# Performance work log

Hardware: AMD Instinct MI355X
Metric: run time of the kernel (lower is better)

## Reference

```python
import jax, jax.numpy as jnp
import numpy as np

NUM_EMBEDDINGS = 1024
EMBEDDING_DIM = 64
COMMITMENT_WEIGHT = 0.25
BATCH = 262144


def setup_inputs() -> dict:
    key = jax.random.key(0)
    k1, k2 = jax.random.split(key)
    z = jax.random.normal(k1, (BATCH, EMBEDDING_DIM), dtype=jnp.float32)
    # torch init: uniform_(-1/K, 1/K)
    bound = 1.0 / NUM_EMBEDDINGS
    codebook = jax.random.uniform(k2, (NUM_EMBEDDINGS, EMBEDDING_DIM), dtype=jnp.float32,
                                  minval=-bound, maxval=bound)
    return {"z": z, "codebook": codebook}


def reference(z, codebook):
    # distances[b, k] = ||z_b||^2 - 2 z_b . c_k + ||c_k||^2   -> [B, K]
    z2 = jnp.sum(z * z, axis=1, keepdims=True)                 # [B, 1]
    c2 = jnp.sum(codebook * codebook, axis=1)                  # [K]
    cross = jnp.matmul(z, codebook.T)                          # [B, K]
    distances = z2 - 2.0 * cross + c2
    indices = jnp.argmin(distances, axis=1)                    # [B]
    # original uses one-hot @ codebook; direct gather is the same math
    z_q = codebook[indices]                                    # [B, D]
    commitment_loss = jnp.mean((jax.lax.stop_gradient(z_q) - z) ** 2)
    codebook_loss = jnp.mean((z_q - jax.lax.stop_gradient(z)) ** 2)
    vq_loss = codebook_loss + COMMITMENT_WEIGHT * commitment_loss
    # straight-through estimator
    z_q_st = z + jax.lax.stop_gradient(z_q - z)
    return z_q_st, vq_loss, indices
```

## Files before the change

### kernel.cpp

```cpp
#include <hip/hip_runtime.h>

#define BATCH   262144
#define NCODE   1024
#define DIM     64
#define BLOCK   256
#define NBLK    (BATCH / BLOCK)
#define MARGIN2 2e-5f
#define QCAP    65536


typedef __attribute__((ext_vector_type(8))) short bf16x8;
typedef __attribute__((ext_vector_type(4))) float f32x4;

#define MFMA(a, b, c) __builtin_amdgcn_mfma_f32_16x16x32_bf16(a, b, c, 0, 0, 0)

__device__ __forceinline__ void split1(float f, unsigned short& h, unsigned short& l) {
    unsigned u = __float_as_uint(f);
    unsigned r = (u + 0x7fffu + ((u >> 16) & 1u)) >> 16;
    h = (unsigned short)r;
    float hf = __uint_as_float(r << 16);
    float lo = f - hf;
    unsigned u2 = __float_as_uint(lo);
    l = (unsigned short)((u2 + 0x7fffu + ((u2 >> 16) & 1u)) >> 16);
}

__global__ __launch_bounds__(256) void prep_kernel(
        const float* __restrict__ cb, float* __restrict__ c2, float* __restrict__ c2n,
        float* __restrict__ cbT, unsigned short* __restrict__ pack,
        unsigned int* __restrict__ qcount)
{
    const int gid = blockIdx.x * 256 + threadIdx.x;
    if (gid == 0) *qcount = 0u;
    cbT[(size_t)(gid & 63) * NCODE + (gid >> 6)] = cb[gid];
    if (gid < NCODE) {
        const float* row = cb + (size_t)gid * DIM;
        float r[8];
#pragma unroll
        for (int j = 0; j < 8; ++j) r[j] = __fmul_rn(row[j], row[j]);
#pragma unroll
        for (int i = 8; i < DIM; i += 8) {
#pragma unroll
            for (int j = 0; j < 8; ++j) r[j] = __fadd_rn(r[j], __fmul_rn(row[i + j], row[i + j]));
        }
        const float v = __fadd_rn(__fadd_rn(__fadd_rn(r[0], r[1]), __fadd_rn(r[2], r[3])),
                                  __fadd_rn(__fadd_rn(r[4], r[5]), __fadd_rn(r[6], r[7])));
        c2[gid] = v;
        c2n[gid] = -0.5f * v;
    }
    if (gid < 4096) {
        const int t = gid >> 6, lane = gid & 63;
        const int c = t * 16 + (lane & 15);
        const int g = lane >> 4;
#pragma unroll
        for (int s = 0; s < 2; ++s) {
            const float* src = cb + (size_t)c * DIM + s * 32 + g * 8;
            bf16x8 hv, lv;
#pragma unroll
            for (int j = 0; j < 8; ++j) {
                unsigned short hh, ll; split1(src[j], hh, ll);
                hv[j] = (short)hh; lv[j] = (short)ll;
            }
            *(bf16x8*)(pack + ((size_t)(t * 4 + 2 * s + 0) * 64 + lane) * 8) = hv;
            *(bf16x8*)(pack + ((size_t)(t * 4 + 2 * s + 1) * 64 + lane) * 8) = lv;
        }
    }
}

__global__ __launch_bounds__(256) void screen_kernel(
        const float* __restrict__ z, const unsigned short* __restrict__ pack,
        const float* __restrict__ c2n, float* __restrict__ out_idx,
        int* __restrict__ queue, unsigned int* __restrict__ qcount)
{
    __shared__ __align__(16) unsigned short lds[2][8192];
    const int tid  = threadIdx.x;
    const int lane = tid & 63, wid = tid >> 6;
    const int col  = lane & 15, g = lane >> 4;
    const int rowbase = blockIdx.x * 128 + wid * 32;

    bf16x8 Ah[2][2], Al[2][2];
#pragma unroll
    for (int rt = 0; rt < 2; ++rt)
#pragma unroll
        for (int s = 0; s < 2; ++s) {
            const float* zp = z + (size_t)(rowbase + rt * 16 + col) * DIM + s * 32 + g * 8;
            float tmp[8];
            *(float4*)(tmp)     = ((const float4*)zp)[0];
            *(float4*)(tmp + 4) = ((const float4*)zp)[1];
            bf16x8 hv, lv;
#pragma unroll
            for (int j = 0; j < 8; ++j) {
                unsigned short hh, ll; split1(tmp[j], hh, ll);
                hv[j] = (short)hh; lv[j] = (short)ll;
            }
            Ah[rt][s] = hv; Al[rt][s] = lv;
        }

    float b1[8], b2[8], bk[8];
#pragma unroll
    for (int i = 0; i < 8; ++i) {
        b1[i] = -__builtin_inff(); b2[i] = -__builtin_inff(); bk[i] = 0.f;
    }
    float codef = (float)col;

#define UPD(i, sv) { const float s_ = (sv); \
                     bk[i] = (s_ > b1[i]) ? codef : bk[i]; \
                     b2[i] = __builtin_amdgcn_fmed3f(s_, b1[i], b2[i]); \
                     b1[i] = fmaxf(b1[i], s_); }

#define STAGE(c, buf) { \
_Pragma("unroll") \
        for (int i_ = 0; i_ < 4; ++i_) { \
            const int seg_ = wid * 4 + i_; \
            const unsigned short* g_ = pack + (size_t)(c) * 8192 + seg_ * 512 + lane * 8; \
            unsigned short* l_ = &lds[buf][seg_ * 512]; \
            __builtin_amdgcn_global_load_lds( \
                (const __attribute__((address_space(1))) unsigned int*)g_, \
                (__attribute__((address_space(3))) unsigned int*)l_, 16, 0, 0); \
        } }

    int cur = 0;
    STAGE(0, 0);
    __syncthreads();
#pragma unroll 1
    for (int c = 0; c < 16; ++c) {
        if (c < 15) STAGE(c + 1, cur ^ 1);
        float c2r[4];
#pragma unroll
        for (int u = 0; u < 4; ++u) c2r[u] = c2n[(c * 4 + u) * 16 + col];
        const unsigned short* buf = &lds[cur][0];
#pragma unroll
        for (int u = 0; u < 4; ++u) {
            const unsigned short* lb = buf + u * 2048;
            bf16x8 Bh0 = *(const bf16x8*)(lb +    0 + lane * 8);
            bf16x8 Bl0 = *(const bf16x8*)(lb +  512 + lane * 8);
            bf16x8 Bh1 = *(const bf16x8*)(lb + 1024 + lane * 8);
            bf16x8 Bl1 = *(const bf16x8*)(lb + 1536 + lane * 8);
            const float cv = c2r[u];
#pragma unroll
            for (int rt = 0; rt < 2; ++rt) {
                f32x4 acc = {cv, cv, cv, cv};
                acc = MFMA(Ah[rt][0], Bh0, acc); acc = MFMA(Ah[rt][1], Bh1, acc);
                acc = MFMA(Ah[rt][0], Bl0, acc); acc = MFMA(Al[rt][0], Bh0, acc);
                acc = MFMA(Ah[rt][1], Bl1, acc); acc = MFMA(Al[rt][1], Bh1, acc);
#pragma unroll
                for (int reg = 0; reg < 4; ++reg) UPD(rt * 4 + reg, acc[reg]);
            }
            codef += 16.f;
        }
        __syncthreads();
        cur ^= 1;
    }
#undef UPD
#undef STAGE

#pragma unroll
    for (int i = 0; i < 8; ++i) {
        float v1 = b1[i], v2 = b2[i], vk = bk[i];
#pragma unroll
        for (int m = 1; m < 16; m <<= 1) {
            const float o1 = __shfl_xor(v1, m);
            const float o2 = __shfl_xor(v2, m);
            const float ok = __shfl_xor(vk, m);
            v2 = fmaxf(fmaxf(v2, o2), fminf(v1, o1));
            if (o1 > v1) vk = ok;
            v1 = fmaxf(v1, o1);
        }
        if (col == 0) {
            const int rt = i >> 2, reg = i & 3;
            const int row = rowbase + rt * 16 + g * 4 + reg;
            out_idx[row] = vk;
            if (v1 - v2 <= MARGIN2) {
                unsigned int p = atomicAdd(qcount, 1u);
                if (p < QCAP) queue[p] = row;
            }
        }
    }
}

__device__ void fix_row(int row, const float* __restrict__ z, const float* __restrict__ cbT,
                        const float* __restrict__ c2, float* __restrict__ out_idx,
                        float* zs, float* rv, int* ri)
{
    const int tid = threadIdx.x;
    __syncthreads();
    if (tid < 16) ((float4*)zs)[tid] = ((const float4*)(z + (size_t)row * DIM))[tid];
    __syncthreads();
    float ra[8];
#pragma unroll
    for (int j = 0; j < 8; ++j) ra[j] = __fmul_rn(zs[j], zs[j]);
#pragma unroll
    for (int d = 8; d < DIM; d += 8) {
#pragma unroll
        for (int j = 0; j < 8; ++j) ra[j] = __fadd_rn(ra[j], __fmul_rn(zs[d + j], zs[d + j]));
    }
    const float z2 = __fadd_rn(__fadd_rn(__fadd_rn(ra[0], ra[1]), __fadd_rn(ra[2], ra[3])),
                               __fadd_rn(__fadd_rn(ra[4], ra[5]), __fadd_rn(ra[6], ra[7])));
    float a[4] = {0.f, 0.f, 0.f, 0.f};
#pragma unroll 8
    for (int d = 0; d < DIM; ++d) {
        const float zd = zs[d];
        const float4 cv = ((const float4*)(cbT + (size_t)d * NCODE))[tid];
        a[0] = __fmaf_rn(zd, cv.x, a[0]);
        a[1] = __fmaf_rn(zd, cv.y, a[1]);
        a[2] = __fmaf_rn(zd, cv.z, a[2]);
        a[3] = __fmaf_rn(zd, cv.w, a[3]);
    }
    const int k0 = tid * 4;
    float best = __builtin_inff();
    int bestk = NCODE;
#pragma unroll
    for (int j = 0; j < 4; ++j) {
        const float dist = __fadd_rn(__fmaf_rn(-2.0f, a[j], z2), c2[k0 + j]);
        if (dist < best) { best = dist; bestk = k0 + j; }
    }
    rv[tid] = best; ri[tid] = bestk;
    __syncthreads();
#pragma unroll
    for (int s = 128; s > 0; s >>= 1) {
        if (tid < s) {
            const float ov = rv[tid + s]; const int oi = ri[tid + s];
            if (ov < rv[tid] || (ov == rv[tid] && oi < ri[tid])) { rv[tid] = ov; ri[tid] = oi; }
        }
        __syncthreads();
    }
    if (tid == 0) out_idx[row] = (float)ri[0];
}

__global__ __launch_bounds__(256) void fix_kernel(
        const float* __restrict__ z, const float* __restrict__ cbT,
        const float* __restrict__ c2, const int* __restrict__ queue,
        const unsigned int* __restrict__ qcount, float* __restrict__ out_idx)
{
    __shared__ float zs[DIM];
    __shared__ float rv[256];
    __shared__ int   ri[256];
    const unsigned int nq = *qcount;
    if (nq <= QCAP) {
        for (unsigned int qi = blockIdx.x; qi < nq; qi += gridDim.x)
            fix_row(queue[qi], z, cbT, c2, out_idx, zs, rv, ri);
    } else {
        for (int row = blockIdx.x; row < BATCH; row += (int)gridDim.x)
            fix_row(row, z, cbT, c2, out_idx, zs, rv, ri);
    }
}

__global__ __launch_bounds__(BLOCK) void emit_kernel(
        const float* __restrict__ z, const float* __restrict__ cb,
        const float* __restrict__ out_idx, float* __restrict__ out_zq,
        double* __restrict__ partial)
{
    const int b = blockIdx.x * BLOCK + threadIdx.x;
    const int bestk = (int)out_idx[b];
    const float* cq = cb + (size_t)bestk * DIM;
    const float4* zv = (const float4*)(z + (size_t)b * DIM);
    const float4* qv = (const float4*)cq;
    float4* ov = (float4*)(out_zq + (size_t)b * DIM);
    double lsum = 0.0;
#pragma unroll
    for (int i = 0; i < DIM / 4; ++i) {
        float4 qq = qv[i], zl = zv[i];
        float qa[4] = {qq.x, qq.y, qq.z, qq.w};
        float za[4] = {zl.x, zl.y, zl.z, zl.w};
        float o[4];
#pragma unroll
        for (int j = 0; j < 4; ++j) {
            const float t = __fsub_rn(qa[j], za[j]);
            o[j] = __fadd_rn(za[j], t);
            lsum += (double)t * (double)t;
        }
        float4 vv; vv.x = o[0]; vv.y = o[1]; vv.z = o[2]; vv.w = o[3];
        ov[i] = vv;
    }

    __shared__ double sred[BLOCK];
    sred[threadIdx.x] = lsum;
    __syncthreads();
#pragma unroll
    for (int s = BLOCK / 2; s > 0; s >>= 1) {
        if (threadIdx.x < s) sred[threadIdx.x] += sred[threadIdx.x + s];
        __syncthreads();
    }
    if (threadIdx.x == 0) partial[blockIdx.x] = sred[0];
}

__global__ void loss_kernel(const double* __restrict__ partial, float* __restrict__ out_loss) {
    __shared__ double sred[256];
    double s = 0.0;
    for (int i = threadIdx.x; i < NBLK; i += 256) s += partial[i];
    sred[threadIdx.x] = s;
    __syncthreads();
#pragma unroll
    for (int st = 128; st > 0; st >>= 1) {
        if (threadIdx.x < st) sred[threadIdx.x] += sred[threadIdx.x + st];
        __syncthreads();
    }
    if (threadIdx.x == 0) {
        const double mean = sred[0] / (double)((size_t)BATCH * DIM);
        const float L = (float)mean;
        out_loss[0] = __fadd_rn(L, __fmul_rn(0.25f, L));
    }
}

extern "C" void kernel_launch(void* const* d_in, const int* in_sizes, int n_in,
                              void* d_out, int out_size, void* d_ws, size_t ws_size,
                              hipStream_t stream) {
    (void)in_sizes; (void)n_in; (void)out_size; (void)ws_size;
    const float* z  = (const float*)d_in[0];
    const float* cb = (const float*)d_in[1];
    float* out      = (float*)d_out;
    float* out_zq   = out;
    float* out_loss = out + (size_t)BATCH * DIM;
    float* out_idx  = out + (size_t)BATCH * DIM + 1;
    double* partial = (double*)d_ws;
    float* c2       = (float*)((char*)d_ws + 8192);
    unsigned int* qcount = (unsigned int*)((char*)d_ws + 12288);
    float* c2n      = (float*)((char*)d_ws + 12544);
    unsigned short* pack = (unsigned short*)((char*)d_ws + 16640);
    int* queue      = (int*)((char*)d_ws + 278784);
    float* cbT      = (float*)((char*)d_ws + 540928);

    prep_kernel<<<256, 256, 0, stream>>>(cb, c2, c2n, cbT, pack, qcount);
    screen_kernel<<<BATCH / 128, 256, 0, stream>>>(z, pack, c2n, out_idx, queue, qcount);
    fix_kernel<<<2048, 256, 0, stream>>>(z, cbT, c2, queue, qcount, out_idx);
    emit_kernel<<<NBLK, BLOCK, 0, stream>>>(z, cb, out_idx, out_zq, partial);
    loss_kernel<<<1, 256, 0, stream>>>(partial, out_loss);
}
```

Before: 307.1 us.

## Stream codebook tiles from global into registers and fuse loss reduction into emit

The screen kernel no longer stages codebook tiles through double-buffered LDS with barriers. Each wave now loads its B fragments straight from global/L2 into registers, ping-ponging between two register sets, and it sets a launch-bounds occupancy hint. The separate loss kernel is removed: emit blocks atomically add their partial sums into a double accumulator, and the last block to finish writes the loss, which saves one launch. This trades LDS traffic and syncs for redundant global reads of the codebook by every wave, and the atomic double summation order becomes nondeterministic.

```diff
diff --git a/kernel.cpp b/kernel.cpp
--- a/kernel.cpp
+++ b/kernel.cpp
@@ -27,10 +27,11 @@
 __global__ __launch_bounds__(256) void prep_kernel(
         const float* __restrict__ cb, float* __restrict__ c2, float* __restrict__ c2n,
         float* __restrict__ cbT, unsigned short* __restrict__ pack,
-        unsigned int* __restrict__ qcount)
+        unsigned int* __restrict__ qcount, double* __restrict__ dsum,
+        unsigned int* __restrict__ dcount)
 {
     const int gid = blockIdx.x * 256 + threadIdx.x;
-    if (gid == 0) *qcount = 0u;
+    if (gid == 0) { *qcount = 0u; *dsum = 0.0; *dcount = 0u; }
     cbT[(size_t)(gid & 63) * NCODE + (gid >> 6)] = cb[gid];
     if (gid < NCODE) {
         const float* row = cb + (size_t)gid * DIM;
@@ -66,12 +67,11 @@
     }
 }
 
-__global__ __launch_bounds__(256) void screen_kernel(
+__global__ __launch_bounds__(256, 4) void screen_kernel(
         const float* __restrict__ z, const unsigned short* __restrict__ pack,
         const float* __restrict__ c2n, float* __restrict__ out_idx,
         int* __restrict__ queue, unsigned int* __restrict__ qcount)
 {
-    __shared__ __align__(16) unsigned short lds[2][8192];
     const int tid  = threadIdx.x;
     const int lane = tid & 63, wid = tid >> 6;
     const int col  = lane & 15, g = lane >> 4;
@@ -107,51 +107,37 @@
                      b2[i] = __builtin_amdgcn_fmed3f(s_, b1[i], b2[i]); \
                      b1[i] = fmaxf(b1[i], s_); }
 
-#define STAGE(c, buf) { \
+#define LOADB(BUF, t) { const unsigned short* p_ = pack + (size_t)(t) * 2048 + lane * 8; \
+        BUF[0] = *(const bf16x8*)(p_);        BUF[1] = *(const bf16x8*)(p_ +  512); \
+        BUF[2] = *(const bf16x8*)(p_ + 1024); BUF[3] = *(const bf16x8*)(p_ + 1536); }
+
+#define COMPUTE(BUF, cv) { \
 _Pragma("unroll") \
-        for (int i_ = 0; i_ < 4; ++i_) { \
-            const int seg_ = wid * 4 + i_; \
-            const unsigned short* g_ = pack + (size_t)(c) * 8192 + seg_ * 512 + lane * 8; \
-            unsigned short* l_ = &lds[buf][seg_ * 512]; \
-            __builtin_amdgcn_global_load_lds( \
-                (const __attribute__((address_space(1))) unsigned int*)g_, \
-                (__attribute__((address_space(3))) unsigned int*)l_, 16, 0, 0); \
-        } }
-
-    int cur = 0;
-    STAGE(0, 0);
-    __syncthreads();
+    for (int rt = 0; rt < 2; ++rt) { \
+        f32x4 acc = {cv, cv, cv, cv}; \
+        acc = MFMA(Ah[rt][0], BUF[0], acc); acc = MFMA(Ah[rt][1], BUF[2], acc); \
+        acc = MFMA(Ah[rt][0], BUF[1], acc); acc = MFMA(Al[rt][0], BUF[0], acc); \
+        acc = MFMA(Ah[rt][1], BUF[3], acc); acc = MFMA(Al[rt][1], BUF[2], acc); \
+_Pragma("unroll") \
+        for (int reg = 0; reg < 4; ++reg) UPD(rt * 4 + reg, acc[reg]); \
+    } \
+    codef += 16.f; }
+
+    bf16x8 BA[4], BB[4];
+    float cA, cB;
+    LOADB(BA, 0); cA = c2n[col];
 #pragma unroll 1
-    for (int c = 0; c < 16; ++c) {
-        if (c < 15) STAGE(c + 1, cur ^ 1);
-        float c2r[4];
-#pragma unroll
-        for (int u = 0; u < 4; ++u) c2r[u] = c2n[(c * 4 + u) * 16 + col];
-        const unsigned short* buf = &lds[cur][0];
-#pragma unroll
-        for (int u = 0; u < 4; ++u) {
-            const unsigned short* lb = buf + u * 2048;
-            bf16x8 Bh0 = *(const bf16x8*)(lb +    0 + lane * 8);
-            bf16x8 Bl0 = *(const bf16x8*)(lb +  512 + lane * 8);
-            bf16x8 Bh1 = *(const bf16x8*)(lb + 1024 + lane * 8);
-            bf16x8 Bl1 = *(const bf16x8*)(lb + 1536 + lane * 8);
-            const float cv = c2r[u];
-#pragma unroll
-            for (int rt = 0; rt < 2; ++rt) {
-                f32x4 acc = {cv, cv, cv, cv};
-                acc = MFMA(Ah[rt][0], Bh0, acc); acc = MFMA(Ah[rt][1], Bh1, acc);
-                acc = MFMA(Ah[rt][0], Bl0, acc); acc = MFMA(Al[rt][0], Bh0, acc);
-                acc = MFMA(Ah[rt][1], Bl1, acc); acc = MFMA(Al[rt][1], Bh1, acc);
-#pragma unroll
-                for (int reg = 0; reg < 4; ++reg) UPD(rt * 4 + reg, acc[reg]);
-            }
-            codef += 16.f;
-        }
-        __syncthreads();
-        cur ^= 1;
-    }
+    for (int tp = 0; tp < 32; ++tp) {
+        const int t1 = 2 * tp + 1;
+        const int t2 = (t1 < 63) ? t1 + 1 : 63;
+        LOADB(BB, t1); cB = c2n[t1 * 16 + col];
+        COMPUTE(BA, cA);
+        LOADB(BA, t2); cA = c2n[t2 * 16 + col];
+        COMPUTE(BB, cB);
+    }
+#undef COMPUTE
+#undef LOADB
 #undef UPD
-#undef STAGE
 
 #pragma unroll
     for (int i = 0; i < 8; ++i) {
@@ -247,7 +233,8 @@
 __global__ __launch_bounds__(BLOCK) void emit_kernel(
         const float* __restrict__ z, const float* __restrict__ cb,
         const float* __restrict__ out_idx, float* __restrict__ out_zq,
-        double* __restrict__ partial)
+        double* __restrict__ dsum, unsigned int* __restrict__ dcount,
+        float* __restrict__ out_loss)
 {
     const int b = blockIdx.x * BLOCK + threadIdx.x;
     const int bestk = (int)out_idx[b];
@@ -280,24 +267,17 @@
         if (threadIdx.x < s) sred[threadIdx.x] += sred[threadIdx.x + s];
         __syncthreads();
     }
-    if (threadIdx.x == 0) partial[blockIdx.x] = sred[0];
-}
-
-__global__ void loss_kernel(const double* __restrict__ partial, float* __restrict__ out_loss) {
-    __shared__ double sred[256];
-    double s = 0.0;
-    for (int i = threadIdx.x; i < NBLK; i += 256) s += partial[i];
-    sred[threadIdx.x] = s;
-    __syncthreads();
-#pragma unroll
-    for (int st = 128; st > 0; st >>= 1) {
-        if (threadIdx.x < st) sred[threadIdx.x] += sred[threadIdx.x + st];
-        __syncthreads();
-    }
     if (threadIdx.x == 0) {
-        const double mean = sred[0] / (double)((size_t)BATCH * DIM);
-        const float L = (float)mean;
-        out_loss[0] = __fadd_rn(L, __fmul_rn(0.25f, L));
+        atomicAdd(dsum, sred[0]);
+        __threadfence();
+        const unsigned int p = atomicAdd(dcount, 1u);
+        if (p == NBLK - 1) {
+            __threadfence();
+            const double tot = atomicAdd(dsum, 0.0);
+            const double mean = tot / (double)((size_t)BATCH * DIM);
+            const float L = (float)mean;
+            out_loss[0] = __fadd_rn(L, __fmul_rn(0.25f, L));
+        }
     }
 }
 
@@ -311,17 +291,17 @@
     float* out_zq   = out;
     float* out_loss = out + (size_t)BATCH * DIM;
     float* out_idx  = out + (size_t)BATCH * DIM + 1;
-    double* partial = (double*)d_ws;
-    float* c2       = (float*)((char*)d_ws + 8192);
-    unsigned int* qcount = (unsigned int*)((char*)d_ws + 12288);
-    float* c2n      = (float*)((char*)d_ws + 12544);
-    unsigned short* pack = (unsigned short*)((char*)d_ws + 16640);
-    int* queue      = (int*)((char*)d_ws + 278784);
-    float* cbT      = (float*)((char*)d_ws + 540928);
-
-    prep_kernel<<<256, 256, 0, stream>>>(cb, c2, c2n, cbT, pack, qcount);
+    double* dsum    = (double*)d_ws;
+    unsigned int* dcount = (unsigned int*)((char*)d_ws + 8);
+    unsigned int* qcount = (unsigned int*)((char*)d_ws + 12);
+    float* c2       = (float*)((char*)d_ws + 1024);
+    float* c2n      = (float*)((char*)d_ws + 5120);
+    unsigned short* pack = (unsigned short*)((char*)d_ws + 16384);
+    int* queue      = (int*)((char*)d_ws + 278528);
+    float* cbT      = (float*)((char*)d_ws + 540672);
+
+    prep_kernel<<<256, 256, 0, stream>>>(cb, c2, c2n, cbT, pack, qcount, dsum, dcount);
     screen_kernel<<<BATCH / 128, 256, 0, stream>>>(z, pack, c2n, out_idx, queue, qcount);
     fix_kernel<<<2048, 256, 0, stream>>>(z, cbT, c2, queue, qcount, out_idx);
-    emit_kernel<<<NBLK, BLOCK, 0, stream>>>(z, cb, out_idx, out_zq, partial);
-    loss_kernel<<<1, 256, 0, stream>>>(partial, out_loss);
-}
+    emit_kernel<<<NBLK, BLOCK, 0, stream>>>(z, cb, out_idx, out_zq, dsum, dcount, out_loss);
+}
```

After: 368.2 us. 1.2x slower.

## Make screen kernel single-wave blocks with per-wave LDS double buffering and no barriers

Applied to the files above, without the earlier changes.

Restructures the screen kernel so each 64-thread block owns 64 rows (4 row tiles per wave) and streams 16-code tiles through a small per-wave double-buffered LDS area. The __syncthreads barriers are replaced by a vmcnt wait, and MFMA sections get raised scheduling priority via s_setprio. This is meant to remove cross-wave barrier stalls and raise the MFMA work per B-fragment load. In exchange it uses more registers for accumulator state, runs more, smaller blocks, and relies on the waitcnt alone to make the async global-to-LDS loads visible before they are read.

```diff
diff --git a/kernel.cpp b/kernel.cpp
--- a/kernel.cpp
+++ b/kernel.cpp
@@ -66,20 +66,19 @@
     }
 }
 
-__global__ __launch_bounds__(256) void screen_kernel(
+__global__ __launch_bounds__(64, 4) void screen_kernel(
         const float* __restrict__ z, const unsigned short* __restrict__ pack,
         const float* __restrict__ c2n, float* __restrict__ out_idx,
         int* __restrict__ queue, unsigned int* __restrict__ qcount)
 {
-    __shared__ __align__(16) unsigned short lds[2][8192];
-    const int tid  = threadIdx.x;
-    const int lane = tid & 63, wid = tid >> 6;
+    __shared__ __align__(16) unsigned short ldsb[2][2048];
+    const int lane = threadIdx.x & 63;
     const int col  = lane & 15, g = lane >> 4;
-    const int rowbase = blockIdx.x * 128 + wid * 32;
-
-    bf16x8 Ah[2][2], Al[2][2];
-#pragma unroll
-    for (int rt = 0; rt < 2; ++rt)
+    const int rowbase = blockIdx.x * 64;
+
+    bf16x8 Ah[4][2], Al[4][2];
+#pragma unroll
+    for (int rt = 0; rt < 4; ++rt)
 #pragma unroll
         for (int s = 0; s < 2; ++s) {
             const float* zp = z + (size_t)(rowbase + rt * 16 + col) * DIM + s * 32 + g * 8;
@@ -95,9 +94,9 @@
             Ah[rt][s] = hv; Al[rt][s] = lv;
         }
 
-    float b1[8], b2[8], bk[8];
-#pragma unroll
-    for (int i = 0; i < 8; ++i) {
+    float b1[16], b2[16], bk[16];
+#pragma unroll
+    for (int i = 0; i < 16; ++i) {
         b1[i] = -__builtin_inff(); b2[i] = -__builtin_inff(); bk[i] = 0.f;
     }
     float codef = (float)col;
@@ -107,54 +106,52 @@
                      b2[i] = __builtin_amdgcn_fmed3f(s_, b1[i], b2[i]); \
                      b1[i] = fmaxf(b1[i], s_); }
 
-#define STAGE(c, buf) { \
+#define STAGE(t, buf) { \
 _Pragma("unroll") \
         for (int i_ = 0; i_ < 4; ++i_) { \
-            const int seg_ = wid * 4 + i_; \
-            const unsigned short* g_ = pack + (size_t)(c) * 8192 + seg_ * 512 + lane * 8; \
-            unsigned short* l_ = &lds[buf][seg_ * 512]; \
+            const unsigned short* g_ = pack + (size_t)(t) * 2048 + i_ * 512 + lane * 8; \
+            unsigned short* l_ = &ldsb[buf][i_ * 512]; \
             __builtin_amdgcn_global_load_lds( \
                 (const __attribute__((address_space(1))) unsigned int*)g_, \
                 (__attribute__((address_space(3))) unsigned int*)l_, 16, 0, 0); \
         } }
 
-    int cur = 0;
     STAGE(0, 0);
-    __syncthreads();
+    float cvc = c2n[col];
 #pragma unroll 1
-    for (int c = 0; c < 16; ++c) {
-        if (c < 15) STAGE(c + 1, cur ^ 1);
-        float c2r[4];
-#pragma unroll
-        for (int u = 0; u < 4; ++u) c2r[u] = c2n[(c * 4 + u) * 16 + col];
-        const unsigned short* buf = &lds[cur][0];
-#pragma unroll
-        for (int u = 0; u < 4; ++u) {
-            const unsigned short* lb = buf + u * 2048;
-            bf16x8 Bh0 = *(const bf16x8*)(lb +    0 + lane * 8);
-            bf16x8 Bl0 = *(const bf16x8*)(lb +  512 + lane * 8);
-            bf16x8 Bh1 = *(const bf16x8*)(lb + 1024 + lane * 8);
-            bf16x8 Bl1 = *(const bf16x8*)(lb + 1536 + lane * 8);
-            const float cv = c2r[u];
-#pragma unroll
-            for (int rt = 0; rt < 2; ++rt) {
-                f32x4 acc = {cv, cv, cv, cv};
-                acc = MFMA(Ah[rt][0], Bh0, acc); acc = MFMA(Ah[rt][1], Bh1, acc);
-                acc = MFMA(Ah[rt][0], Bl0, acc); acc = MFMA(Al[rt][0], Bh0, acc);
-                acc = MFMA(Ah[rt][1], Bl1, acc); acc = MFMA(Al[rt][1], Bh1, acc);
-#pragma unroll
-                for (int reg = 0; reg < 4; ++reg) UPD(rt * 4 + reg, acc[reg]);
-            }
-            codef += 16.f;
-        }
-        __syncthreads();
-        cur ^= 1;
+    for (int t = 0; t < 64; ++t) {
+        const int cur = t & 1;
+        asm volatile("s_waitcnt vmcnt(0)" ::: "memory");
+        const unsigned short* lb = &ldsb[cur][0];
+        bf16x8 B0 = *(const bf16x8*)(lb +    0 + lane * 8);
+        bf16x8 B1 = *(const bf16x8*)(lb +  512 + lane * 8);
+        bf16x8 B2 = *(const bf16x8*)(lb + 1024 + lane * 8);
+        bf16x8 B3 = *(const bf16x8*)(lb + 1536 + lane * 8);
+        float cvn = 0.f;
+        if (t < 63) {
+            STAGE(t + 1, cur ^ 1);
+            cvn = c2n[(t + 1) * 16 + col];
+        }
+        const float cv = cvc;
+        __builtin_amdgcn_s_setprio(1);
+#pragma unroll
+        for (int rt = 0; rt < 4; ++rt) {
+            f32x4 acc = {cv, cv, cv, cv};
+            acc = MFMA(Ah[rt][0], B0, acc); acc = MFMA(Ah[rt][1], B2, acc);
+            acc = MFMA(Ah[rt][0], B1, acc); acc = MFMA(Al[rt][0], B0, acc);
+            acc = MFMA(Ah[rt][1], B3, acc); acc = MFMA(Al[rt][1], B2, acc);
+#pragma unroll
+            for (int reg = 0; reg < 4; ++reg) UPD(rt * 4 + reg, acc[reg]);
+        }
+        __builtin_amdgcn_s_setprio(0);
+        cvc = cvn;
+        codef += 16.f;
     }
 #undef UPD
 #undef STAGE
 
 #pragma unroll
-    for (int i = 0; i < 8; ++i) {
+    for (int i = 0; i < 16; ++i) {
         float v1 = b1[i], v2 = b2[i], vk = bk[i];
 #pragma unroll
         for (int m = 1; m < 16; m <<= 1) {
@@ -320,7 +317,7 @@
     float* cbT      = (float*)((char*)d_ws + 540928);
 
     prep_kernel<<<256, 256, 0, stream>>>(cb, c2, c2n, cbT, pack, qcount);
-    screen_kernel<<<BATCH / 128, 256, 0, stream>>>(z, pack, c2n, out_idx, queue, qcount);
+    screen_kernel<<<BATCH / 64, 64, 0, stream>>>(z, pack, c2n, out_idx, queue, qcount);
     fix_kernel<<<2048, 256, 0, stream>>>(z, cbT, c2, queue, qcount, out_idx);
     emit_kernel<<<NBLK, BLOCK, 0, stream>>>(z, cb, out_idx, out_zq, partial);
     loss_kernel<<<1, 256, 0, stream>>>(partial, out_loss);
```

Result: slower. 448.0 us (+45.8%).
